# Optimization experiments

Hardware: AMD Instinct MI355X
Metric: run time of the kernel (lower is better)

## Reference

```python
import jax, jax.numpy as jnp
import numpy as np

N_NODES = 50000
N_EDGES = 800000
IN_C, HID_C, OUT_C = 96, 64, 40
ALPHA = 0.2
K = 2
NEG_SLOPE = 0.01  # F.leaky_relu default


def setup_inputs() -> dict:
    key = jax.random.key(0)
    k_x, k_e, k_w0, k_b0, k_w4, k_b4 = jax.random.split(key, 6)
    x = jax.random.normal(k_x, (N_NODES, IN_C), dtype=jnp.float32)
    edge_index = jax.random.randint(k_e, (2, N_EDGES), 0, N_NODES, dtype=jnp.int64)
    # SGConv linear layers (torch.nn.Linear layout: [out, in])
    W0 = jax.random.normal(k_w0, (HID_C, IN_C), dtype=jnp.float32) / np.sqrt(IN_C)
    b0 = jax.random.normal(k_b0, (HID_C,), dtype=jnp.float32) * 0.01
    W4 = jax.random.normal(k_w4, (OUT_C, HID_C), dtype=jnp.float32) / np.sqrt(HID_C)
    b4 = jax.random.normal(k_b4, (OUT_C,), dtype=jnp.float32) * 0.01
    return {"x": x, "edge_index": edge_index, "W0": W0, "b0": b0, "W4": W4, "b4": b4}


def reference(x, edge_index, W0, b0, W4, b4):
    # GCN normalization with self-loops (shared by SGConv and APPNP in PyG):
    # A_hat = A + I, prop(h) = D^{-1/2} A_hat D^{-1/2} h
    n = x.shape[0]
    loops = jnp.arange(n, dtype=edge_index.dtype)
    src = jnp.concatenate([edge_index[0], loops])
    dst = jnp.concatenate([edge_index[1], loops])
    deg = jax.ops.segment_sum(jnp.ones_like(dst, dtype=x.dtype), dst, num_segments=n)
    dinv = jnp.where(deg > 0, jax.lax.rsqrt(deg), 0.0)
    norm = dinv[src] * dinv[dst]  # [E + N]

    def prop(h):
        # gather -> scale -> scatter-add  (irregular memory-bound core op)
        return jax.ops.segment_sum(norm[:, None] * h[src], dst, num_segments=n)

    def sg_prop(h):  # SGConv: K propagation steps, then linear
        for _ in range(K):
            h = prop(h)
        return h

    def appnp(h0):  # APPNP: z_{k+1} = (1-alpha) * prop(z_k) + alpha * h0
        z = h0
        for _ in range(K):
            z = (1.0 - ALPHA) * prop(z) + ALPHA * h0
        return z

    h = sg_prop(x) @ W0.T + b0          # conv0 (SGConv)
    # dropout is identity in eval mode (training=False)
    h = jax.nn.leaky_relu(appnp(h), NEG_SLOPE)   # conv1
    h = jax.nn.leaky_relu(appnp(h), NEG_SLOPE)   # conv2
    h = jax.nn.leaky_relu(appnp(h), NEG_SLOPE)   # conv3
    h = sg_prop(h) @ W4.T + b4          # conv4 (SGConv)
    return jax.nn.log_softmax(h, axis=1)
```

## Files before the change

### kernel.cpp

```cpp
#include <hip/hip_runtime.h>
#include <hip/hip_fp16.h>
#include <math.h>

#define N_NODES 50000
#define N_EDGES 800000
#define IN_C 96
#define HID_C 64
#define OUT_C 40
#define ALPHA 0.2f
#define NEG_SLOPE 0.01f
#define QCAP 131072

typedef _Float16 f16x8 __attribute__((ext_vector_type(8)));
typedef float f32x4 __attribute__((ext_vector_type(4)));

__device__ __forceinline__ int edge_at(const void* ei, int is64, long long pos) {
    return is64 ? (int)((const long long*)ei)[pos] : ((const int*)ei)[pos];
}

__global__ void zero_detect_k(int* deg, int n, int* qtail, const unsigned int* ei, int* flag) {
    int i = blockIdx.x * blockDim.x + threadIdx.x;
    if (i < n) deg[i] = 0;
    if (i < 8) qtail[i] = 0;
    if (i == 0) {
        int is64 = 1;
        for (int j = 1; j < 16; j += 2)
            if (ei[j] != 0u) is64 = 0;
        *flag = is64;
    }
}

__global__ void bucketA_k(const void* ei, const int* flag, int* __restrict__ deg,
                          int* __restrict__ qtail, int2* __restrict__ queue, int E) {
    __shared__ int cnt[8], qb[8];
    int f = *flag;
    int e0 = blockIdx.x * 1024;
    if (threadIdx.x < 8) cnt[threadIdx.x] = 0;
    __syncthreads();
    int s[4], d[4], p[4], r[4];
    #pragma unroll
    for (int k = 0; k < 4; ++k) {
        int e = e0 + threadIdx.x + k * 256;
        if (e < E) {
            d[k] = edge_at(ei, f, (long long)E + e);
            s[k] = edge_at(ei, f, e);
            atomicAdd(&deg[d[k]], 1);
            p[k] = d[k] / (N_NODES / 8);
            if (p[k] > 7) p[k] = 7;
            r[k] = atomicAdd(&cnt[p[k]], 1);
        } else p[k] = -1;
    }
    __syncthreads();
    if (threadIdx.x < 8) qb[threadIdx.x] = atomicAdd(&qtail[threadIdx.x], cnt[threadIdx.x]);
    __syncthreads();
    #pragma unroll
    for (int k = 0; k < 4; ++k) {
        if (p[k] >= 0) {
            int pos = qb[p[k]] + r[k];
            if (pos < QCAP) queue[(size_t)p[k] * QCAP + pos] = make_int2(s[k], d[k]);
        }
    }
}

__global__ void bucketB_k(const int* __restrict__ qtail, const int2* __restrict__ queue,
                          int* __restrict__ cursor, int* __restrict__ csrc) {
    int p = blockIdx.x & 7;
    int j = blockIdx.x >> 3;
    int J = gridDim.x >> 3;
    int n = qtail[p]; if (n > QCAP) n = QCAP;
    const int2* q = queue + (size_t)p * QCAP;
    for (int i = j * blockDim.x + threadIdx.x; i < n; i += J * blockDim.x) {
        int2 e = q[i];
        int pos = atomicAdd(&cursor[e.y], 1);
        csrc[pos] = e.x;
    }
}

__global__ void scan_p1_k(const int* __restrict__ deg, int* __restrict__ part, int n) {
    __shared__ int sm[256];
    int t = threadIdx.x, i = blockIdx.x * 256 + t;
    int v = (i < n) ? deg[i] : 0;
    sm[t] = v;
    __syncthreads();
    for (int off = 1; off < 256; off <<= 1) {
        int u = (t >= off) ? sm[t - off] : 0;
        __syncthreads();
        sm[t] += u;
        __syncthreads();
    }
    if (t == 255) part[blockIdx.x] = sm[255];
}

__global__ void scan_p2_k(int* part, int nb, int* rowptr, int n) {
    __shared__ int sm[256];
    int t = threadIdx.x;
    int v = (t < nb) ? part[t] : 0;
    sm[t] = v;
    __syncthreads();
    for (int off = 1; off < 256; off <<= 1) {
        int u = (t >= off) ? sm[t - off] : 0;
        __syncthreads();
        sm[t] += u;
        __syncthreads();
    }
    if (t < nb) part[t] = sm[t] - v;
    if (t == 255) rowptr[n] = sm[255];
}

__global__ void scan_p3_k(const int* __restrict__ deg, const int* __restrict__ part,
                          int* __restrict__ rowptr, int* __restrict__ cursor,
                          float* __restrict__ dinv, int* __restrict__ bcnt, int n) {
    __shared__ int sm[256];
    __shared__ int h[64];
    int t = threadIdx.x, i = blockIdx.x * 256 + t;
    if (t < 64) h[t] = 0;
    int v = (i < n) ? deg[i] : 0;
    sm[t] = v;
    __syncthreads();
    for (int off = 1; off < 256; off <<= 1) {
        int u = (t >= off) ? sm[t - off] : 0;
        __syncthreads();
        sm[t] += u;
        __syncthreads();
    }
    if (i < n) {
        int excl = sm[t] - v + part[blockIdx.x];
        rowptr[i] = excl;
        cursor[i] = excl;
        dinv[i] = rsqrtf((float)v + 1.0f);
        int dd = v; if (dd > 63) dd = 63;
        atomicAdd(&h[63 - dd], 1);
    }
    __syncthreads();
    if (t < 64) bcnt[blockIdx.x * 64 + t] = h[t];
}

__global__ void bscanA_k(const int* __restrict__ bcnt, int* __restrict__ bbase,
                         int* __restrict__ tot, int nb) {
    __shared__ int sm[256];
    int b = blockIdx.x;
    int t = threadIdx.x;
    int v = (t < nb) ? bcnt[t * 64 + b] : 0;
    sm[t] = v;
    __syncthreads();
    for (int off = 1; off < 256; off <<= 1) {
        int u = (t >= off) ? sm[t - off] : 0;
        __syncthreads();
        sm[t] += u;
        __syncthreads();
    }
    if (t < nb) bbase[t * 64 + b] = sm[t] - v;
    if (t == 255) tot[b] = sm[255];
}

__global__ void perm_k(const int* __restrict__ deg, const int* __restrict__ bbase,
                       const int* __restrict__ tot, int* __restrict__ perm, int n) {
    __shared__ int h[64], bs[64];
    int t = threadIdx.x, i = blockIdx.x * 256 + t;
    if (t < 64) { h[t] = 0; bs[t] = tot[t]; }
    __syncthreads();
    if (t == 0) {
        int run = 0;
        for (int k = 0; k < 64; ++k) { int v = bs[k]; bs[k] = run; run += v; }
    }
    __syncthreads();
    if (i < n) {
        int d = deg[i]; if (d > 63) d = 63;
        int b = 63 - d;
        int rank = atomicAdd(&h[b], 1);
        perm[bs[b] + bbase[blockIdx.x * 64 + b] + rank] = i;
    }
}

__device__ __forceinline__ void add8(float* acc, float4 v, float w) {
    const __half2* hp = (const __half2*)&v;
    #pragma unroll
    for (int j = 0; j < 4; ++j) {
        float2 f = __half22float2(hp[j]);
        acc[2 * j] += w * f.x;
        acc[2 * j + 1] += w * f.y;
    }
}

template <bool COMBINE, bool LEAKY, bool BIAS>
__global__ void __launch_bounds__(256) prop64_k(
        const int* __restrict__ perm,
        const int* __restrict__ rowptr, const int* __restrict__ csrc,
        const float* __restrict__ dinv,
        const __half* __restrict__ in, const __half* __restrict__ h0,
        const float* __restrict__ bias,
        __half* __restrict__ out, int N) {
    int g = blockIdx.x * (blockDim.x >> 3) + (threadIdx.x >> 3);
    int ci = threadIdx.x & 7;
    if (g >= N) return;
    int node = perm[g];
    const float4* in8 = (const float4*)in;
    float acc[8];
    {
        float4 r = in8[node * 8 + ci];
        const __half2* hp = (const __half2*)&r;
        #pragma unroll
        for (int j = 0; j < 4; ++j) {
            float2 f = __half22float2(hp[j]);
            acc[2 * j] = f.x;
            acc[2 * j + 1] = f.y;
        }
    }
    int r0 = rowptr[node], r1 = rowptr[node + 1];
    int i = r0;
    int s[8];
    if (i + 7 < r1) {
        #pragma unroll
        for (int j = 0; j < 8; ++j) s[j] = csrc[i + j];
    }
    for (; i + 15 < r1; i += 8) {
        float4 v[8];
        #pragma unroll
        for (int j = 0; j < 8; ++j) v[j] = in8[(size_t)s[j] * 8 + ci];
        #pragma unroll
        for (int j = 0; j < 8; ++j) s[j] = csrc[i + 8 + j];
        #pragma unroll
        for (int j = 0; j < 8; ++j) add8(acc, v[j], 1.0f);
    }
    if (i + 7 < r1) {
        float4 v[8];
        #pragma unroll
        for (int j = 0; j < 8; ++j) v[j] = in8[(size_t)s[j] * 8 + ci];
        #pragma unroll
        for (int j = 0; j < 8; ++j) add8(acc, v[j], 1.0f);
        i += 8;
    }
    for (; i + 3 < r1; i += 4) {
        int s0 = csrc[i], s1 = csrc[i + 1], s2 = csrc[i + 2], s3 = csrc[i + 3];
        float4 v0 = in8[(size_t)s0 * 8 + ci];
        float4 v1 = in8[(size_t)s1 * 8 + ci];
        float4 v2 = in8[(size_t)s2 * 8 + ci];
        float4 v3 = in8[(size_t)s3 * 8 + ci];
        add8(acc, v0, 1.0f);
        add8(acc, v1, 1.0f);
        add8(acc, v2, 1.0f);
        add8(acc, v3, 1.0f);
    }
    for (; i < r1; ++i) {
        float4 v0 = in8[(size_t)csrc[i] * 8 + ci];
        add8(acc, v0, 1.0f);
    }
    float di = dinv[node];
    float sc = di * di;
    float v[8];
    #pragma unroll
    for (int j = 0; j < 8; ++j) v[j] = sc * acc[j];
    if (BIAS) {
        float4 b0v = ((const float4*)bias)[2 * ci];
        float4 b1v = ((const float4*)bias)[2 * ci + 1];
        v[0] += di * b0v.x; v[1] += di * b0v.y; v[2] += di * b0v.z; v[3] += di * b0v.w;
        v[4] += di * b1v.x; v[5] += di * b1v.y; v[6] += di * b1v.z; v[7] += di * b1v.w;
    }
    if (COMBINE) {
        float4 r = ((const float4*)h0)[node * 8 + ci];
        const __half2* hp = (const __half2*)&r;
        #pragma unroll
        for (int j = 0; j < 4; ++j) {
            float2 f = __half22float2(hp[j]);
            v[2 * j]     = (1.0f - ALPHA) * v[2 * j]     + ALPHA * f.x;
            v[2 * j + 1] = (1.0f - ALPHA) * v[2 * j + 1] + ALPHA * f.y;
        }
    }
    if (LEAKY) {
        #pragma unroll
        for (int j = 0; j < 8; ++j) v[j] = v[j] > 0.0f ? v[j] : NEG_SLOPE * v[j];
    }
    float4 o;
    __half2* op = (__half2*)&o;
    #pragma unroll
    for (int j = 0; j < 4; ++j)
        op[j] = __float22half2_rn(make_float2(v[2 * j], v[2 * j + 1]));
    ((float4*)out)[node * 8 + ci] = o;
}

__global__ void __launch_bounds__(256) prop40_k(
        const int* __restrict__ perm,
        const int* __restrict__ rowptr, const int* __restrict__ csrc,
        const float* __restrict__ dinv,
        const __half* __restrict__ in, __half* __restrict__ out, int N) {
    int g = blockIdx.x * (blockDim.x >> 3) + (threadIdx.x >> 3);
    int ci = threadIdx.x & 7;
    if (g >= N) return;
    int node = perm[g];
    bool act = ci < 5;
    int cc = act ? ci : 0;
    const float4* in4 = (const float4*)in;
    float acc[8];
    {
        float4 r = in4[(size_t)node * 8 + cc];
        const __half2* hp = (const __half2*)&r;
        #pragma unroll
        for (int j = 0; j < 4; ++j) {
            float2 f = __half22float2(hp[j]);
            acc[2 * j] = f.x;
            acc[2 * j + 1] = f.y;
        }
    }
    int r0 = rowptr[node], r1 = rowptr[node + 1];
    int i = r0;
    int s[8];
    if (i + 7 < r1) {
        #pragma unroll
        for (int j = 0; j < 8; ++j) s[j] = csrc[i + j];
    }
    for (; i + 15 < r1; i += 8) {
        float4 v[8];
        #pragma unroll
        for (int j = 0; j < 8; ++j) v[j] = in4[(size_t)s[j] * 8 + cc];
        #pragma unroll
        for (int j = 0; j < 8; ++j) s[j] = csrc[i + 8 + j];
        #pragma unroll
        for (int j = 0; j < 8; ++j) add8(acc, v[j], 1.0f);
    }
    if (i + 7 < r1) {
        float4 v[8];
        #pragma unroll
        for (int j = 0; j < 8; ++j) v[j] = in4[(size_t)s[j] * 8 + cc];
        #pragma unroll
        for (int j = 0; j < 8; ++j) add8(acc, v[j], 1.0f);
        i += 8;
    }
    for (; i + 3 < r1; i += 4) {
        int s0 = csrc[i], s1 = csrc[i + 1], s2 = csrc[i + 2], s3 = csrc[i + 3];
        float4 v0 = in4[(size_t)s0 * 8 + cc];
        float4 v1 = in4[(size_t)s1 * 8 + cc];
        float4 v2 = in4[(size_t)s2 * 8 + cc];
        float4 v3 = in4[(size_t)s3 * 8 + cc];
        add8(acc, v0, 1.0f);
        add8(acc, v1, 1.0f);
        add8(acc, v2, 1.0f);
        add8(acc, v3, 1.0f);
    }
    for (; i < r1; ++i) {
        float4 v0 = in4[(size_t)csrc[i] * 8 + cc];
        add8(acc, v0, 1.0f);
    }
    if (act) {
        float di = dinv[node];
        float sc = di * di;
        float4 o;
        __half2* op = (__half2*)&o;
        #pragma unroll
        for (int j = 0; j < 4; ++j)
            op[j] = __float22half2_rn(make_float2(sc * acc[2 * j], sc * acc[2 * j + 1]));
        ((float4*)out)[(size_t)node * 8 + ci] = o;
    }
}

__global__ void __launch_bounds__(256) prop40_softmax_k(
        const int* __restrict__ perm,
        const int* __restrict__ rowptr, const int* __restrict__ csrc,
        const float* __restrict__ dinv,
        const __half* __restrict__ in, const float* __restrict__ bias,
        float* __restrict__ out, int N) {
    int g = blockIdx.x * (blockDim.x >> 3) + (threadIdx.x >> 3);
    int ci = threadIdx.x & 7;
    if (g >= N) return;
    int node = perm[g];
    bool act = ci < 5;
    int cc = act ? ci : 0;
    const float4* in4 = (const float4*)in;
    float acc[8];
    {
        float4 r = in4[(size_t)node * 8 + cc];
        const __half2* hp = (const __half2*)&r;
        #pragma unroll
        for (int j = 0; j < 4; ++j) {
            float2 f = __half22float2(hp[j]);
            acc[2 * j] = f.x;
            acc[2 * j + 1] = f.y;
        }
    }
    int r0 = rowptr[node], r1 = rowptr[node + 1];
    int i = r0;
    int s[8];
    if (i + 7 < r1) {
        #pragma unroll
        for (int j = 0; j < 8; ++j) s[j] = csrc[i + j];
    }
    for (; i + 15 < r1; i += 8) {
        float4 v[8];
        #pragma unroll
        for (int j = 0; j < 8; ++j) v[j] = in4[(size_t)s[j] * 8 + cc];
        #pragma unroll
        for (int j = 0; j < 8; ++j) s[j] = csrc[i + 8 + j];
        #pragma unroll
        for (int j = 0; j < 8; ++j) add8(acc, v[j], 1.0f);
    }
    if (i + 7 < r1) {
        float4 v[8];
        #pragma unroll
        for (int j = 0; j < 8; ++j) v[j] = in4[(size_t)s[j] * 8 + cc];
        #pragma unroll
        for (int j = 0; j < 8; ++j) add8(acc, v[j], 1.0f);
        i += 8;
    }
    for (; i + 3 < r1; i += 4) {
        int s0 = csrc[i], s1 = csrc[i + 1], s2 = csrc[i + 2], s3 = csrc[i + 3];
        float4 v0 = in4[(size_t)s0 * 8 + cc];
        float4 v1 = in4[(size_t)s1 * 8 + cc];
        float4 v2 = in4[(size_t)s2 * 8 + cc];
        float4 v3 = in4[(size_t)s3 * 8 + cc];
        add8(acc, v0, 1.0f);
        add8(acc, v1, 1.0f);
        add8(acc, v2, 1.0f);
        add8(acc, v3, 1.0f);
    }
    for (; i < r1; ++i) {
        float4 v0 = in4[(size_t)csrc[i] * 8 + cc];
        add8(acc, v0, 1.0f);
    }
    float di = dinv[node];
    float v[8];
    if (act) {
        float4 b0v = ((const float4*)bias)[2 * ci];
        float4 b1v = ((const float4*)bias)[2 * ci + 1];
        v[0] = di * acc[0] + b0v.x; v[1] = di * acc[1] + b0v.y;
        v[2] = di * acc[2] + b0v.z; v[3] = di * acc[3] + b0v.w;
        v[4] = di * acc[4] + b1v.x; v[5] = di * acc[5] + b1v.y;
        v[6] = di * acc[6] + b1v.z; v[7] = di * acc[7] + b1v.w;
    } else {
        #pragma unroll
        for (int j = 0; j < 8; ++j) v[j] = -INFINITY;
    }
    float m = v[0];
    #pragma unroll
    for (int j = 1; j < 8; ++j) m = fmaxf(m, v[j]);
    #pragma unroll
    for (int off = 4; off >= 1; off >>= 1) m = fmaxf(m, __shfl_xor(m, off));
    float e = 0.0f;
    if (act) {
        #pragma unroll
        for (int j = 0; j < 8; ++j) e += expf(v[j] - m);
    }
    #pragma unroll
    for (int off = 4; off >= 1; off >>= 1) e += __shfl_xor(e, off);
    float ls = m + logf(e);
    if (act) {
        float4 o0 = make_float4(v[0] - ls, v[1] - ls, v[2] - ls, v[3] - ls);
        float4 o1 = make_float4(v[4] - ls, v[5] - ls, v[6] - ls, v[7] - ls);
        ((float4*)out)[(size_t)node * 10 + 2 * ci] = o0;
        ((float4*)out)[(size_t)node * 10 + 2 * ci + 1] = o1;
    }
}

template <int O, int K, int OP, bool FP32IN, bool SCALE>
__global__ void __launch_bounds__(256) mfma_lin_k(const void* __restrict__ in_,
                                                  const float* __restrict__ W,
                                                  const float* __restrict__ dinv,
                                                  __half* __restrict__ out, int Mtiles) {
    constexpr int P2 = 52;
    __shared__ __half2 wsh[O * P2];
    for (int idx = threadIdx.x; idx < O * (K / 2); idx += 256) {
        int o = idx / (K / 2), kk = idx - o * (K / 2);
        float2 w2 = ((const float2*)W)[o * (K / 2) + kk];
        wsh[o * P2 + kk] = __floats2half2_rn(w2.x, w2.y);
    }
    __syncthreads();
    int wave = (blockIdx.x * 256 + threadIdx.x) >> 6;
    if (wave >= Mtiles) return;
    int lane = threadIdx.x & 63;
    int lm = lane & 15, q = lane >> 4;
    long long m0 = (long long)wave * 16;
    constexpr int NT = (O + 15) / 16;
    f32x4 acc[NT];
    #pragma unroll
    for (int j = 0; j < NT; ++j) acc[j] = (f32x4){0.f, 0.f, 0.f, 0.f};
    const __half* wsp = (const __half*)wsh;
    #pragma unroll
    for (int k0 = 0; k0 < K; k0 += 32) {
        f16x8 a;
        if (FP32IN) {
            const float* xr = (const float*)in_ + (m0 + lm) * K + k0 + q * 8;
            float4 x0 = ((const float4*)xr)[0];
            float4 x1 = ((const float4*)xr)[1];
            a = (f16x8){(_Float16)x0.x, (_Float16)x0.y, (_Float16)x0.z, (_Float16)x0.w,
                        (_Float16)x1.x, (_Float16)x1.y, (_Float16)x1.z, (_Float16)x1.w};
        } else {
            const __half* xr = (const __half*)in_ + (m0 + lm) * K + k0 + q * 8;
            a = *(const f16x8*)xr;
        }
        #pragma unroll
        for (int j = 0; j < NT; ++j) {
            f16x8 b = *(const f16x8*)(wsp + (16 * j + lm) * (2 * P2) + k0 + q * 8);
            acc[j] = __builtin_amdgcn_mfma_f32_16x16x32_f16(a, b, acc[j], 0, 0, 0);
        }
    }
    #pragma unroll
    for (int r = 0; r < 4; ++r) {
        long long m = m0 + q * 4 + r;
        float sc = SCALE ? dinv[m] : 1.0f;
        #pragma unroll
        for (int j = 0; j < NT; ++j) {
            int col = 16 * j + lm;
            if (col < OP) out[m * OP + col] = __float2half(acc[j][r] * sc);
        }
    }
}

static inline int cdiv(long long a, long long b) { return (int)((a + b - 1) / b); }
static inline size_t align256(size_t x) { return (x + 255) & ~(size_t)255; }

extern "C" void kernel_launch(void* const* d_in, const int* in_sizes, int n_in,
                              void* d_out, int out_size, void* d_ws, size_t ws_size,
                              hipStream_t stream) {
    const float* x  = (const float*)d_in[0];
    const void*  ei = d_in[1];
    const float* W0 = (const float*)d_in[2];
    const float* b0 = (const float*)d_in[3];
    const float* W4 = (const float*)d_in[4];
    const float* b4 = (const float*)d_in[5];
    float* out = (float*)d_out;

    const int N = N_NODES, E = N_EDGES;
    const int NB = cdiv(N, 256);
    char* ws = (char*)d_ws;
    int*    flag   = (int*)ws;     ws += 256;
    int*    deg    = (int*)ws;     ws += align256((size_t)N * 4);
    int*    rowptr = (int*)ws;     ws += align256((size_t)(N + 1) * 4);
    int*    cursor = (int*)ws;     ws += align256((size_t)N * 4);
    int*    part   = (int*)ws;     ws += align256(256 * 4);
    int*    bcnt   = (int*)ws;     ws += align256((size_t)NB * 64 * 4);
    int*    bbase  = (int*)ws;     ws += align256((size_t)NB * 64 * 4);
    int*    tot    = (int*)ws;     ws += align256(64 * 4);
    int*    qtail  = (int*)ws;     ws += align256(8 * 4);
    int*    perm   = (int*)ws;     ws += align256((size_t)N * 4);
    float*  dinv   = (float*)ws;   ws += align256((size_t)N * 4);
    int*    csrc   = (int*)ws;     ws += align256((size_t)E * 4);
    int2*   queue  = (int2*)ws;    ws += align256((size_t)8 * QCAP * 8);
    __half* bufA   = (__half*)ws;  ws += align256((size_t)N * HID_C * 2);
    __half* bufB   = (__half*)ws;  ws += align256((size_t)N * HID_C * 2);
    __half* bufC   = (__half*)ws;  ws += align256((size_t)N * HID_C * 2);

    const int T = 256;
    const int MT = N / 16;
    const int LB = cdiv(MT, 4);
    const int P64B = cdiv(N, T / 8);
    const int P40B = cdiv(N, T / 8);

    zero_detect_k<<<cdiv(N, T), T, 0, stream>>>(deg, N, qtail, (const unsigned int*)ei, flag);
    bucketA_k<<<cdiv(E, 1024), T, 0, stream>>>(ei, flag, deg, qtail, queue, E);
    scan_p1_k<<<NB, 256, 0, stream>>>(deg, part, N);
    scan_p2_k<<<1, 256, 0, stream>>>(part, NB, rowptr, N);
    scan_p3_k<<<NB, 256, 0, stream>>>(deg, part, rowptr, cursor, dinv, bcnt, N);
    bscanA_k<<<64, 256, 0, stream>>>(bcnt, bbase, tot, NB);
    perm_k<<<NB, 256, 0, stream>>>(deg, bbase, tot, perm, N);
    bucketB_k<<<8 * 64, T, 0, stream>>>(qtail, queue, cursor, csrc);

    mfma_lin_k<HID_C, IN_C, HID_C, true, true><<<LB, 256, 0, stream>>>(x, W0, dinv, bufA, MT);
    prop64_k<false, false, false><<<P64B, T, 0, stream>>>(
        perm, rowptr, csrc, dinv, bufA, nullptr, nullptr, bufB, N);
    prop64_k<false, false, true><<<P64B, T, 0, stream>>>(
        perm, rowptr, csrc, dinv, bufB, nullptr, b0, bufC, N);

    for (int r = 0; r < 3; ++r) {
        prop64_k<true, false, false><<<P64B, T, 0, stream>>>(
            perm, rowptr, csrc, dinv, bufC, bufC, nullptr, bufB, N);
        prop64_k<true, true, false><<<P64B, T, 0, stream>>>(
            perm, rowptr, csrc, dinv, bufB, bufC, nullptr, bufC, N);
    }

    mfma_lin_k<OUT_C, HID_C, HID_C, false, false><<<LB, 256, 0, stream>>>(
        bufC, W4, dinv, bufA, MT);
    prop40_k<<<P40B, T, 0, stream>>>(perm, rowptr, csrc, dinv, bufA, bufB, N);
    prop40_softmax_k<<<P40B, T, 0, stream>>>(perm, rowptr, csrc, dinv, bufB, b4, out, N);
}
```

Before: 333.9 us.

## Fuse eight 64-channel propagation launches into one cooperative persistent kernel

Replaces the eight separate prop64 kernel launches with a single cooperative kernel. A grid-stride loop runs each propagation step, and grid.sync() separates the steps. Buffers now rotate through three slots (A, B, C) so the APPNP h0 input stays valid, and the later linear and prop40 stages are rewired to match. The aim is to remove per-launch overhead and tail gaps between steps. The trade-off is that grid size is capped by occupancy, which can reduce latency hiding for the irregular gather, and each grid-wide barrier has its own cost. It also changes the mfma_lin store guard from OP to O.

```diff
diff --git a/kernel.cpp b/kernel.cpp
--- a/kernel.cpp
+++ b/kernel.cpp
@@ -1,6 +1,9 @@
 #include <hip/hip_runtime.h>
 #include <hip/hip_fp16.h>
+#include <hip/hip_cooperative_groups.h>
 #include <math.h>
+
+namespace cg = cooperative_groups;
 
 #define N_NODES 50000
 #define N_EDGES 800000
@@ -13,6 +16,12 @@
 
 typedef _Float16 f16x8 __attribute__((ext_vector_type(8)));
 typedef float f32x4 __attribute__((ext_vector_type(4)));
+
+struct GP {
+    const float* b0;
+    int* rowptr; int* perm; float* dinv; int* csrc;
+    __half* bufA; __half* bufB; __half* bufC;
+};
 
 __device__ __forceinline__ int edge_at(const void* ei, int is64, long long pos) {
     return is64 ? (int)((const long long*)ei)[pos] : ((const int*)ei)[pos];
@@ -172,41 +181,28 @@
     }
 }
 
-__device__ __forceinline__ void add8(float* acc, float4 v, float w) {
+__device__ __forceinline__ void add8(float* acc, float4 v) {
     const __half2* hp = (const __half2*)&v;
     #pragma unroll
     for (int j = 0; j < 4; ++j) {
         float2 f = __half22float2(hp[j]);
-        acc[2 * j] += w * f.x;
-        acc[2 * j + 1] += w * f.y;
-    }
-}
-
-template <bool COMBINE, bool LEAKY, bool BIAS>
-__global__ void __launch_bounds__(256) prop64_k(
-        const int* __restrict__ perm,
-        const int* __restrict__ rowptr, const int* __restrict__ csrc,
-        const float* __restrict__ dinv,
-        const __half* __restrict__ in, const __half* __restrict__ h0,
-        const float* __restrict__ bias,
-        __half* __restrict__ out, int N) {
-    int g = blockIdx.x * (blockDim.x >> 3) + (threadIdx.x >> 3);
-    int ci = threadIdx.x & 7;
-    if (g >= N) return;
-    int node = perm[g];
-    const float4* in8 = (const float4*)in;
-    float acc[8];
-    {
-        float4 r = in8[node * 8 + ci];
-        const __half2* hp = (const __half2*)&r;
-        #pragma unroll
-        for (int j = 0; j < 4; ++j) {
-            float2 f = __half22float2(hp[j]);
-            acc[2 * j] = f.x;
-            acc[2 * j + 1] = f.y;
-        }
-    }
-    int r0 = rowptr[node], r1 = rowptr[node + 1];
+        acc[2 * j] += f.x;
+        acc[2 * j + 1] += f.y;
+    }
+}
+
+__device__ __forceinline__ void unpack8(float* acc, float4 r) {
+    const __half2* hp = (const __half2*)&r;
+    #pragma unroll
+    for (int j = 0; j < 4; ++j) {
+        float2 f = __half22float2(hp[j]);
+        acc[2 * j] = f.x;
+        acc[2 * j + 1] = f.y;
+    }
+}
+
+__device__ __forceinline__ void gather8(const float4* __restrict__ in8, int ci,
+        const int* __restrict__ csrc, int r0, int r1, float* acc) {
     int i = r0;
     int s[8];
     if (i + 7 < r1) {
@@ -220,14 +216,14 @@
         #pragma unroll
         for (int j = 0; j < 8; ++j) s[j] = csrc[i + 8 + j];
         #pragma unroll
-        for (int j = 0; j < 8; ++j) add8(acc, v[j], 1.0f);
+        for (int j = 0; j < 8; ++j) add8(acc, v[j]);
     }
     if (i + 7 < r1) {
         float4 v[8];
         #pragma unroll
         for (int j = 0; j < 8; ++j) v[j] = in8[(size_t)s[j] * 8 + ci];
         #pragma unroll
-        for (int j = 0; j < 8; ++j) add8(acc, v[j], 1.0f);
+        for (int j = 0; j < 8; ++j) add8(acc, v[j]);
         i += 8;
     }
     for (; i + 3 < r1; i += 4) {
@@ -236,46 +232,62 @@
         float4 v1 = in8[(size_t)s1 * 8 + ci];
         float4 v2 = in8[(size_t)s2 * 8 + ci];
         float4 v3 = in8[(size_t)s3 * 8 + ci];
-        add8(acc, v0, 1.0f);
-        add8(acc, v1, 1.0f);
-        add8(acc, v2, 1.0f);
-        add8(acc, v3, 1.0f);
-    }
-    for (; i < r1; ++i) {
-        float4 v0 = in8[(size_t)csrc[i] * 8 + ci];
-        add8(acc, v0, 1.0f);
-    }
-    float di = dinv[node];
-    float sc = di * di;
-    float v[8];
-    #pragma unroll
-    for (int j = 0; j < 8; ++j) v[j] = sc * acc[j];
-    if (BIAS) {
-        float4 b0v = ((const float4*)bias)[2 * ci];
-        float4 b1v = ((const float4*)bias)[2 * ci + 1];
-        v[0] += di * b0v.x; v[1] += di * b0v.y; v[2] += di * b0v.z; v[3] += di * b0v.w;
-        v[4] += di * b1v.x; v[5] += di * b1v.y; v[6] += di * b1v.z; v[7] += di * b1v.w;
-    }
-    if (COMBINE) {
-        float4 r = ((const float4*)h0)[node * 8 + ci];
-        const __half2* hp = (const __half2*)&r;
-        #pragma unroll
-        for (int j = 0; j < 4; ++j) {
-            float2 f = __half22float2(hp[j]);
-            v[2 * j]     = (1.0f - ALPHA) * v[2 * j]     + ALPHA * f.x;
-            v[2 * j + 1] = (1.0f - ALPHA) * v[2 * j + 1] + ALPHA * f.y;
-        }
-    }
-    if (LEAKY) {
-        #pragma unroll
-        for (int j = 0; j < 8; ++j) v[j] = v[j] > 0.0f ? v[j] : NEG_SLOPE * v[j];
-    }
-    float4 o;
-    __half2* op = (__half2*)&o;
-    #pragma unroll
-    for (int j = 0; j < 4; ++j)
-        op[j] = __float22half2_rn(make_float2(v[2 * j], v[2 * j + 1]));
-    ((float4*)out)[node * 8 + ci] = o;
+        add8(acc, v0); add8(acc, v1); add8(acc, v2); add8(acc, v3);
+    }
+    for (; i < r1; ++i) add8(acc, in8[(size_t)csrc[i] * 8 + ci]);
+}
+
+template <int MODE>
+__device__ void prop64_body(const GP& p, const __half* __restrict__ in,
+                            const __half* __restrict__ h0, __half* __restrict__ out, int G) {
+    int grp = threadIdx.x >> 3, ci = threadIdx.x & 7;
+    const float4* in8 = (const float4*)in;
+    for (int g = blockIdx.x * 32 + grp; g < N_NODES; g += G * 32) {
+        int node = p.perm[g];
+        int r0 = p.rowptr[node], r1 = p.rowptr[node + 1];
+        float di = p.dinv[node];
+        float acc[8];
+        unpack8(acc, in8[(size_t)node * 8 + ci]);
+        gather8(in8, ci, p.csrc, r0, r1, acc);
+        float sc = di * di;
+        float v[8];
+        #pragma unroll
+        for (int j = 0; j < 8; ++j) v[j] = sc * acc[j];
+        if (MODE == 1) {
+            float4 b0v = ((const float4*)p.b0)[2 * ci];
+            float4 b1v = ((const float4*)p.b0)[2 * ci + 1];
+            v[0] += di * b0v.x; v[1] += di * b0v.y; v[2] += di * b0v.z; v[3] += di * b0v.w;
+            v[4] += di * b1v.x; v[5] += di * b1v.y; v[6] += di * b1v.z; v[7] += di * b1v.w;
+        }
+        if (MODE >= 2) {
+            float h[8];
+            unpack8(h, ((const float4*)h0)[(size_t)node * 8 + ci]);
+            #pragma unroll
+            for (int j = 0; j < 8; ++j) v[j] = (1.0f - ALPHA) * v[j] + ALPHA * h[j];
+        }
+        if (MODE == 3) {
+            #pragma unroll
+            for (int j = 0; j < 8; ++j) v[j] = v[j] > 0.0f ? v[j] : NEG_SLOPE * v[j];
+        }
+        float4 o;
+        __half2* op = (__half2*)&o;
+        #pragma unroll
+        for (int j = 0; j < 4; ++j)
+            op[j] = __float22half2_rn(make_float2(v[2 * j], v[2 * j + 1]));
+        ((float4*)out)[(size_t)node * 8 + ci] = o;
+    }
+}
+
+__global__ void __launch_bounds__(256) prop_core_k(GP p, int G) {
+    cg::grid_group grid = cg::this_grid();
+    prop64_body<0>(p, p.bufA, nullptr, p.bufB, G); grid.sync();
+    prop64_body<1>(p, p.bufB, nullptr, p.bufC, G); grid.sync();
+    prop64_body<2>(p, p.bufC, p.bufC, p.bufB, G);  grid.sync();
+    prop64_body<3>(p, p.bufB, p.bufC, p.bufA, G);  grid.sync();
+    prop64_body<2>(p, p.bufA, p.bufA, p.bufB, G);  grid.sync();
+    prop64_body<3>(p, p.bufB, p.bufA, p.bufC, G);  grid.sync();
+    prop64_body<2>(p, p.bufC, p.bufC, p.bufB, G);  grid.sync();
+    prop64_body<3>(p, p.bufB, p.bufC, p.bufA, G);
 }
 
 __global__ void __launch_bounds__(256) prop40_k(
@@ -291,55 +303,9 @@
     int cc = act ? ci : 0;
     const float4* in4 = (const float4*)in;
     float acc[8];
-    {
-        float4 r = in4[(size_t)node * 8 + cc];
-        const __half2* hp = (const __half2*)&r;
-        #pragma unroll
-        for (int j = 0; j < 4; ++j) {
-            float2 f = __half22float2(hp[j]);
-            acc[2 * j] = f.x;
-            acc[2 * j + 1] = f.y;
-        }
-    }
+    unpack8(acc, in4[(size_t)node * 8 + cc]);
     int r0 = rowptr[node], r1 = rowptr[node + 1];
-    int i = r0;
-    int s[8];
-    if (i + 7 < r1) {
-        #pragma unroll
-        for (int j = 0; j < 8; ++j) s[j] = csrc[i + j];
-    }
-    for (; i + 15 < r1; i += 8) {
-        float4 v[8];
-        #pragma unroll
-        for (int j = 0; j < 8; ++j) v[j] = in4[(size_t)s[j] * 8 + cc];
-        #pragma unroll
-        for (int j = 0; j < 8; ++j) s[j] = csrc[i + 8 + j];
-        #pragma unroll
-        for (int j = 0; j < 8; ++j) add8(acc, v[j], 1.0f);
-    }
-    if (i + 7 < r1) {
-        float4 v[8];
-        #pragma unroll
-        for (int j = 0; j < 8; ++j) v[j] = in4[(size_t)s[j] * 8 + cc];
-        #pragma unroll
-        for (int j = 0; j < 8; ++j) add8(acc, v[j], 1.0f);
-        i += 8;
-    }
-    for (; i + 3 < r1; i += 4) {
-        int s0 = csrc[i], s1 = csrc[i + 1], s2 = csrc[i + 2], s3 = csrc[i + 3];
-        float4 v0 = in4[(size_t)s0 * 8 + cc];
-        float4 v1 = in4[(size_t)s1 * 8 + cc];
-        float4 v2 = in4[(size_t)s2 * 8 + cc];
-        float4 v3 = in4[(size_t)s3 * 8 + cc];
-        add8(acc, v0, 1.0f);
-        add8(acc, v1, 1.0f);
-        add8(acc, v2, 1.0f);
-        add8(acc, v3, 1.0f);
-    }
-    for (; i < r1; ++i) {
-        float4 v0 = in4[(size_t)csrc[i] * 8 + cc];
-        add8(acc, v0, 1.0f);
-    }
+    gather8(in4, cc, csrc, r0, r1, acc);
     if (act) {
         float di = dinv[node];
         float sc = di * di;
@@ -366,55 +332,9 @@
     int cc = act ? ci : 0;
     const float4* in4 = (const float4*)in;
     float acc[8];
-    {
-        float4 r = in4[(size_t)node * 8 + cc];
-        const __half2* hp = (const __half2*)&r;
-        #pragma unroll
-        for (int j = 0; j < 4; ++j) {
-            float2 f = __half22float2(hp[j]);
-            acc[2 * j] = f.x;
-            acc[2 * j + 1] = f.y;
-        }
-    }
+    unpack8(acc, in4[(size_t)node * 8 + cc]);
     int r0 = rowptr[node], r1 = rowptr[node + 1];
-    int i = r0;
-    int s[8];
-    if (i + 7 < r1) {
-        #pragma unroll
-        for (int j = 0; j < 8; ++j) s[j] = csrc[i + j];
-    }
-    for (; i + 15 < r1; i += 8) {
-        float4 v[8];
-        #pragma unroll
-        for (int j = 0; j < 8; ++j) v[j] = in4[(size_t)s[j] * 8 + cc];
-        #pragma unroll
-        for (int j = 0; j < 8; ++j) s[j] = csrc[i + 8 + j];
-        #pragma unroll
-        for (int j = 0; j < 8; ++j) add8(acc, v[j], 1.0f);
-    }
-    if (i + 7 < r1) {
-        float4 v[8];
-        #pragma unroll
-        for (int j = 0; j < 8; ++j) v[j] = in4[(size_t)s[j] * 8 + cc];
-        #pragma unroll
-        for (int j = 0; j < 8; ++j) add8(acc, v[j], 1.0f);
-        i += 8;
-    }
-    for (; i + 3 < r1; i += 4) {
-        int s0 = csrc[i], s1 = csrc[i + 1], s2 = csrc[i + 2], s3 = csrc[i + 3];
-        float4 v0 = in4[(size_t)s0 * 8 + cc];
-        float4 v1 = in4[(size_t)s1 * 8 + cc];
-        float4 v2 = in4[(size_t)s2 * 8 + cc];
-        float4 v3 = in4[(size_t)s3 * 8 + cc];
-        add8(acc, v0, 1.0f);
-        add8(acc, v1, 1.0f);
-        add8(acc, v2, 1.0f);
-        add8(acc, v3, 1.0f);
-    }
-    for (; i < r1; ++i) {
-        float4 v0 = in4[(size_t)csrc[i] * 8 + cc];
-        add8(acc, v0, 1.0f);
-    }
+    gather8(in4, cc, csrc, r0, r1, acc);
     float di = dinv[node];
     float v[8];
     if (act) {
@@ -498,7 +418,7 @@
         #pragma unroll
         for (int j = 0; j < NT; ++j) {
             int col = 16 * j + lm;
-            if (col < OP) out[m * OP + col] = __float2half(acc[j][r] * sc);
+            if (col < O) out[m * OP + col] = __float2half(acc[j][r] * sc);
         }
     }
 }
@@ -540,8 +460,12 @@
     const int T = 256;
     const int MT = N / 16;
     const int LB = cdiv(MT, 4);
-    const int P64B = cdiv(N, T / 8);
     const int P40B = cdiv(N, T / 8);
+
+    GP p;
+    p.b0 = b0;
+    p.rowptr = rowptr; p.perm = perm; p.dinv = dinv; p.csrc = csrc;
+    p.bufA = bufA; p.bufB = bufB; p.bufC = bufC;
 
     zero_detect_k<<<cdiv(N, T), T, 0, stream>>>(deg, N, qtail, (const unsigned int*)ei, flag);
     bucketA_k<<<cdiv(E, 1024), T, 0, stream>>>(ei, flag, deg, qtail, queue, E);
@@ -553,20 +477,18 @@
     bucketB_k<<<8 * 64, T, 0, stream>>>(qtail, queue, cursor, csrc);
 
     mfma_lin_k<HID_C, IN_C, HID_C, true, true><<<LB, 256, 0, stream>>>(x, W0, dinv, bufA, MT);
-    prop64_k<false, false, false><<<P64B, T, 0, stream>>>(
-        perm, rowptr, csrc, dinv, bufA, nullptr, nullptr, bufB, N);
-    prop64_k<false, false, true><<<P64B, T, 0, stream>>>(
-        perm, rowptr, csrc, dinv, bufB, nullptr, b0, bufC, N);
-
-    for (int r = 0; r < 3; ++r) {
-        prop64_k<true, false, false><<<P64B, T, 0, stream>>>(
-            perm, rowptr, csrc, dinv, bufC, bufC, nullptr, bufB, N);
-        prop64_k<true, true, false><<<P64B, T, 0, stream>>>(
-            perm, rowptr, csrc, dinv, bufB, bufC, nullptr, bufC, N);
-    }
+
+    int occ = 0;
+    if (hipOccupancyMaxActiveBlocksPerMultiprocessor(&occ, prop_core_k, 256, 0)
+            != hipSuccess || occ < 1) occ = 4;
+    int G = cdiv(N, 32);
+    int cap = occ * 256;
+    if (G > cap) G = cap;
+    void* args[] = { &p, &G };
+    hipLaunchCooperativeKernel((void*)prop_core_k, dim3(G), dim3(256), args, 0, stream);
 
     mfma_lin_k<OUT_C, HID_C, HID_C, false, false><<<LB, 256, 0, stream>>>(
-        bufC, W4, dinv, bufA, MT);
-    prop40_k<<<P40B, T, 0, stream>>>(perm, rowptr, csrc, dinv, bufA, bufB, N);
+        bufA, W4, dinv, bufC, MT);
+    prop40_k<<<P40B, T, 0, stream>>>(perm, rowptr, csrc, dinv, bufC, bufB, N);
     prop40_softmax_k<<<P40B, T, 0, stream>>>(perm, rowptr, csrc, dinv, bufB, b4, out, N);
 }
```

After: 821.6 us. +146.0%, slower.
